# Kernel tuning notes

Measured on AMD Instinct MI355X. Metric: run time of the kernel, lower is better.

Reference implementation:

```python
import jax, jax.numpy as jnp
import numpy as np

NUM_JOINT = 19
BATCH = 262144
ROOT_SCALE = 200.0
# Topologically-ordered humanoid skeleton: parent[j] < j for all non-root joints.
# 0: hips, 1-4: spine/head chain, 5-8: left arm, 9-12: right arm, 13-15: left leg, 16-18: right leg
PARENTS = np.array([-1, 0, 1, 2, 3, 2, 5, 6, 7, 2, 9, 10, 11, 0, 13, 14, 0, 16, 17], dtype=np.int32)


def quaternion_to_matrix(q):
    # q: [..., 4] in (w, x, y, z) order (pytorch3d convention, non-unit tolerant)
    w, x, y, z = q[..., 0], q[..., 1], q[..., 2], q[..., 3]
    two_s = 2.0 / jnp.sum(q * q, axis=-1)
    r = jnp.stack([
        1.0 - two_s * (y * y + z * z), two_s * (x * y - z * w), two_s * (x * z + y * w),
        two_s * (x * y + z * w), 1.0 - two_s * (x * x + z * z), two_s * (y * z - x * w),
        two_s * (x * z - y * w), two_s * (y * z + x * w), 1.0 - two_s * (x * x + y * y),
    ], axis=-1)
    return r.reshape(q.shape[:-1] + (3, 3))


def setup_inputs() -> dict:
    key = jax.random.key(0)
    k1, k2, k3 = jax.random.split(key, 3)
    root_position = jax.random.normal(k1, (BATCH, 3), dtype=jnp.float32)
    joint = jax.random.normal(k2, (BATCH, NUM_JOINT * 4), dtype=jnp.float32)
    # Homogeneous translation matrices per bone: identity rotation, translation in column 3.
    trans = jax.random.normal(k3, (NUM_JOINT, 3), dtype=jnp.float32) * 10.0
    offsets = jnp.tile(jnp.eye(4, dtype=jnp.float32)[None], (NUM_JOINT, 1, 1))
    offsets = offsets.at[:, :3, 3].set(trans)
    return {"root_position": root_position, "joint": joint, "offsets": offsets}


def reference(root_position, joint, offsets):
    B = joint.shape[0]
    q = joint.reshape(B, NUM_JOINT, 4)
    R3 = quaternion_to_matrix(q)  # [B, J, 3, 3]
    R4 = jnp.zeros((B, NUM_JOINT, 4, 4), dtype=joint.dtype)
    R4 = R4.at[:, :, :3, :3].set(R3).at[:, :, 3, 3].set(1.0)
    # RT = rotation @ bone offset, batched over all joints at once
    RT = jnp.einsum('bjik,jkl->bjil', R4, offsets)  # [B, J, 4, 4]
    # Sequential parent-child chain over the (small, fixed) skeleton tree
    mats = [RT[:, 0]]
    for j in range(1, NUM_JOINT):
        mats.append(jnp.matmul(mats[PARENTS[j]], RT[:, j]))
    M = jnp.stack(mats, axis=1)  # [B, J, 4, 4] world transforms
    # joint position = column 3 of the homogeneous transform (== transpose row 3 in source)
    pos = M[:, :, :, 3]  # [B, J, 4]
    pos = pos.at[:, :, :3].add((root_position * ROOT_SCALE)[:, None, :])
    return pos
```

## Files before the change

kernel.cpp:

```cpp
#include <hip/hip_runtime.h>

#define NJ 19
#define ROOT_SCALE 200.0f
#define BLOCK 128
#define ROWF 76
#define ROWV 19
#define STRIDE 84

struct Xform { float r[9]; float t[3]; };

__device__ __forceinline__ void quat_rt(float w, float x, float y, float z,
                                        float tx, float ty, float tz, Xform& o) {
    float ts = 2.0f / (w*w + x*x + y*y + z*z);
    o.r[0] = 1.0f - ts*(y*y + z*z); o.r[1] = ts*(x*y - z*w);        o.r[2] = ts*(x*z + y*w);
    o.r[3] = ts*(x*y + z*w);        o.r[4] = 1.0f - ts*(x*x + z*z); o.r[5] = ts*(y*z - x*w);
    o.r[6] = ts*(x*z - y*w);        o.r[7] = ts*(y*z + x*w);        o.r[8] = 1.0f - ts*(x*x + y*y);
    o.t[0] = o.r[0]*tx + o.r[1]*ty + o.r[2]*tz;
    o.t[1] = o.r[3]*tx + o.r[4]*ty + o.r[5]*tz;
    o.t[2] = o.r[6]*tx + o.r[7]*ty + o.r[8]*tz;
}

__device__ __forceinline__ void compose(const Xform& p, const Xform& l, Xform& o) {
#pragma unroll
    for (int i = 0; i < 3; ++i) {
        o.r[i*3+0] = p.r[i*3+0]*l.r[0] + p.r[i*3+1]*l.r[3] + p.r[i*3+2]*l.r[6];
        o.r[i*3+1] = p.r[i*3+0]*l.r[1] + p.r[i*3+1]*l.r[4] + p.r[i*3+2]*l.r[7];
        o.r[i*3+2] = p.r[i*3+0]*l.r[2] + p.r[i*3+1]*l.r[5] + p.r[i*3+2]*l.r[8];
        o.t[i]     = p.r[i*3+0]*l.t[0] + p.r[i*3+1]*l.t[1] + p.r[i*3+2]*l.t[2] + p.t[i];
    }
}

__global__ __launch_bounds__(BLOCK) void fk_kernel(
    const float* __restrict__ root, const float* __restrict__ joint,
    const float* __restrict__ offs, float* __restrict__ out, int batch)
{
    __shared__ float s[BLOCK * STRIDE];
    const int tid = threadIdx.x;
    const int rowBase = blockIdx.x * BLOCK;
    const long long gbase = (long long)rowBase * ROWF;
    const int nvalid = min(BLOCK, batch - rowBase);

    if (nvalid == BLOCK) {
#pragma unroll
        for (int i = 0; i < ROWV; ++i) {
            int v = i * BLOCK + tid;
            int r = v / ROWV;
            int c = (v - r * ROWV) * 4;
            float4 val = *(const float4*)(joint + gbase + (long long)v * 4);
            *(float4*)(&s[r * STRIDE + c]) = val;
        }
    } else {
        for (int v = tid; v < nvalid * ROWV; v += BLOCK) {
            int r = v / ROWV;
            int c = (v - r * ROWV) * 4;
            float4 val = *(const float4*)(joint + gbase + (long long)v * 4);
            *(float4*)(&s[r * STRIDE + c]) = val;
        }
    }
    __syncthreads();

    if (tid < nvalid) {
        float* row = &s[tid * STRIDE];
        const int b = rowBase + tid;
        const float rx = root[(long long)b*3 + 0] * ROOT_SCALE;
        const float ry = root[(long long)b*3 + 1] * ROOT_SCALE;
        const float rz = root[(long long)b*3 + 2] * ROOT_SCALE;

        Xform cur, sv0, sv2, loc;
#pragma unroll
        for (int j = 0; j < NJ; ++j) {
            float4 q = *(const float4*)(&row[j*4]);
            float tx = offs[j*16 + 3], ty = offs[j*16 + 7], tz = offs[j*16 + 11];
            quat_rt(q.x, q.y, q.z, q.w, tx, ty, tz, loc);
            if (j == 0) {
                cur = loc;
            } else {
                Xform nxt;
                if (j == 5 || j == 9)        compose(sv2, loc, nxt);
                else if (j == 13 || j == 16) compose(sv0, loc, nxt);
                else                         compose(cur, loc, nxt);
                cur = nxt;
            }
            if (j == 0) sv0 = cur;
            if (j == 2) sv2 = cur;
            float4 o;
            o.x = cur.t[0] + rx;
            o.y = cur.t[1] + ry;
            o.z = cur.t[2] + rz;
            o.w = 1.0f;
            *(float4*)(&row[j*4]) = o;
        }
    }
    __syncthreads();

    if (nvalid == BLOCK) {
#pragma unroll
        for (int i = 0; i < ROWV; ++i) {
            int v = i * BLOCK + tid;
            int r = v / ROWV;
            int c = (v - r * ROWV) * 4;
            *(float4*)(out + gbase + (long long)v * 4) = *(const float4*)(&s[r * STRIDE + c]);
        }
    } else {
        for (int v = tid; v < nvalid * ROWV; v += BLOCK) {
            int r = v / ROWV;
            int c = (v - r * ROWV) * 4;
            *(float4*)(out + gbase + (long long)v * 4) = *(const float4*)(&s[r * STRIDE + c]);
        }
    }
}

extern "C" void kernel_launch(void* const* d_in, const int* in_sizes, int n_in,
                              void* d_out, int out_size, void* d_ws, size_t ws_size,
                              hipStream_t stream) {
    const float* root  = (const float*)d_in[0];
    const float* joint = (const float*)d_in[1];
    const float* offs  = (const float*)d_in[2];
    float* out = (float*)d_out;
    const int batch = in_sizes[1] / ROWF;
    const int grid = (batch + BLOCK - 1) / BLOCK;
    fk_kernel<<<grid, BLOCK, 0, stream>>>(root, joint, offs, out, batch);
}
```

Measured before the change: 152.7 us.

## Stage joint rows into LDS via direct global_load_lds and drop padding

Replaces the register-staged global-to-LDS copy with the AMD global_load_lds builtin (16-byte direct-to-LDS loads). The shared buffer becomes unpadded with a contiguous row layout, which removes the divide-by-19 index math. Block size drops from 128 to 64 with a launch-bounds occupancy hint. In exchange, rows are now laid out with a 76-float stride, which may cause LDS bank conflicts on the per-thread row reads and writes, and the 16-byte direct-to-LDS load needs hardware support (gfx950).

```diff
diff --git a/kernel.cpp b/kernel.cpp
--- a/kernel.cpp
+++ b/kernel.cpp
@@ -1,11 +1,11 @@
 #include <hip/hip_runtime.h>
+#include <stdint.h>
 
 #define NJ 19
 #define ROOT_SCALE 200.0f
-#define BLOCK 128
+#define BLOCK 64
 #define ROWF 76
 #define ROWV 19
-#define STRIDE 84
 
 struct Xform { float r[9]; float t[3]; };
 
@@ -30,11 +30,11 @@
     }
 }
 
-__global__ __launch_bounds__(BLOCK) void fk_kernel(
+__global__ __launch_bounds__(BLOCK, 2) void fk_kernel(
     const float* __restrict__ root, const float* __restrict__ joint,
     const float* __restrict__ offs, float* __restrict__ out, int batch)
 {
-    __shared__ float s[BLOCK * STRIDE];
+    __shared__ float s[BLOCK * ROWF];
     const int tid = threadIdx.x;
     const int rowBase = blockIdx.x * BLOCK;
     const long long gbase = (long long)rowBase * ROWF;
@@ -43,24 +43,22 @@
     if (nvalid == BLOCK) {
 #pragma unroll
         for (int i = 0; i < ROWV; ++i) {
-            int v = i * BLOCK + tid;
-            int r = v / ROWV;
-            int c = (v - r * ROWV) * 4;
-            float4 val = *(const float4*)(joint + gbase + (long long)v * 4);
-            *(float4*)(&s[r * STRIDE + c]) = val;
+            __builtin_amdgcn_global_load_lds(
+                (const __attribute__((address_space(1))) uint32_t*)
+                    (joint + gbase + (long long)(i * BLOCK + tid) * 4),
+                (__attribute__((address_space(3))) uint32_t*)(s + i * BLOCK * 4),
+                16, 0, 0);
         }
     } else {
         for (int v = tid; v < nvalid * ROWV; v += BLOCK) {
-            int r = v / ROWV;
-            int c = (v - r * ROWV) * 4;
-            float4 val = *(const float4*)(joint + gbase + (long long)v * 4);
-            *(float4*)(&s[r * STRIDE + c]) = val;
+            *(float4*)(s + 4 * v) =
+                *(const float4*)(joint + gbase + (long long)v * 4);
         }
     }
     __syncthreads();
 
     if (tid < nvalid) {
-        float* row = &s[tid * STRIDE];
+        float* row = s + tid * ROWF;
         const int b = rowBase + tid;
         const float rx = root[(long long)b*3 + 0] * ROOT_SCALE;
         const float ry = root[(long long)b*3 + 1] * ROOT_SCALE;
@@ -97,15 +95,11 @@
 #pragma unroll
         for (int i = 0; i < ROWV; ++i) {
             int v = i * BLOCK + tid;
-            int r = v / ROWV;
-            int c = (v - r * ROWV) * 4;
-            *(float4*)(out + gbase + (long long)v * 4) = *(const float4*)(&s[r * STRIDE + c]);
+            *(float4*)(out + gbase + (long long)v * 4) = *(const float4*)(s + 4 * v);
         }
     } else {
         for (int v = tid; v < nvalid * ROWV; v += BLOCK) {
-            int r = v / ROWV;
-            int c = (v - r * ROWV) * 4;
-            *(float4*)(out + gbase + (long long)v * 4) = *(const float4*)(&s[r * STRIDE + c]);
+            *(float4*)(out + gbase + (long long)v * 4) = *(const float4*)(s + 4 * v);
         }
     }
 }
```

New measurement: 151.1 us. Within noise of the previous version (-1.0%).
